# Kernel optimization log

Measured on AMD Instinct MI355X. Metric: run time of the kernel, lower is better.

## Reference

```python
import jax, jax.numpy as jnp
import numpy as np

B, L, C, H = 8, 1024, 384, 6
D = C // H          # head_dim = 64
K, N = 2, 4         # radial_degree, angular_degree
EPS = 1e-5


def setup_inputs() -> dict:
    key = jax.random.key(0)
    ks = jax.random.split(key, 8)
    x = jax.random.normal(ks[0], (B, L, C), dtype=jnp.float32)
    pos = jax.random.uniform(ks[1], (B, L, 2), dtype=jnp.float32) * 32.0
    w_norm = jnp.ones((C,), dtype=jnp.float32)
    w_in = jax.random.normal(ks[2], (3 * C, C), dtype=jnp.float32) * 0.02
    b_in = jnp.zeros((3 * C,), dtype=jnp.float32)
    w_out = jax.random.normal(ks[3], (C, C), dtype=jnp.float32) * 0.02
    b_out = jnp.zeros((C,), dtype=jnp.float32)
    b_coef = jax.random.normal(ks[4], (H, K + 1, N + 1), dtype=jnp.float32) * 0.01
    b_coef = b_coef.at[:, 1, 0].set(1.0)  # reset_parameters fills b[..., 1, 0] = 1
    c_coef = jax.random.normal(ks[5], (H, K + 1, N + 1), dtype=jnp.float32) * 0.01
    return {"x": x, "pos": pos, "w_norm": w_norm, "w_in": w_in, "b_in": b_in,
            "w_out": w_out, "b_out": b_out, "b_coef": b_coef, "c_coef": c_coef}


def _polar_bias(pos, b_coef, c_coef):
    # pos: (B, L, 2) -> bias grid (B, H, L, L)
    dist = pos[:, :, None, :] - pos[:, None, :, :]           # (B, Lq, Lk, 2)
    theta = jnp.arctan2(dist[..., 1], dist[..., 0])          # (B, Lq, Lk)
    r = jnp.sqrt(jnp.sum(dist * dist, axis=-1))              # (B, Lq, Lk)
    r_pow = r[..., None] ** jnp.arange(K + 1, dtype=r.dtype)           # (B, Lq, Lk, K+1)
    ang = theta[..., None] * jnp.arange(N + 1, dtype=theta.dtype)      # (B, Lq, Lk, N+1)
    cos_part = jnp.einsum('hkn,bijk,bijn->bhij', b_coef, r_pow, jnp.cos(ang))
    sin_part = jnp.einsum('hkn,bijk,bijn->bhij', c_coef, r_pow, jnp.sin(ang))
    return cos_part + sin_part


def reference(x, pos, w_norm, w_in, b_in, w_out, b_out, b_coef, c_coef):
    # RMSNorm
    ms = jnp.mean(x * x, axis=-1, keepdims=True)
    xn = x * jax.lax.rsqrt(ms + EPS) * w_norm
    # packed QKV projection
    qkv = xn @ w_in.T + b_in                                  # (B, L, 3C)
    q, k, v = jnp.split(qkv, 3, axis=-1)
    def heads(t):  # (B, L, C) -> (B, H, L, D)
        return t.reshape(B, L, H, D).transpose(0, 2, 1, 3)
    q, k, v = heads(q), heads(k), heads(v)
    bias = _polar_bias(pos, b_coef, c_coef)                   # (B, H, L, L)
    scores = jnp.einsum('bhqd,bhkd->bhqk', q, k) / jnp.sqrt(jnp.float32(D)) + bias
    attn = jax.nn.softmax(scores, axis=-1)
    o = jnp.einsum('bhqk,bhkd->bhqd', attn, v)                # (B, H, L, D)
    o = o.transpose(0, 2, 1, 3).reshape(B, L, C)
    return o @ w_out.T + b_out
```

## Files before the change

### kernel.cpp

```cpp
#include <hip/hip_runtime.h>

typedef unsigned int  u32;
typedef unsigned short u16;
typedef __attribute__((ext_vector_type(8))) short short8;
typedef __attribute__((ext_vector_type(4))) float f32x4;

__device__ __forceinline__ u16 f2bf(float x) {
  union { float f; u32 u; } un; un.f = x;
  u32 r = un.u + 0x7FFFu + ((un.u >> 16) & 1u);
  return (u16)(r >> 16);
}
__device__ __forceinline__ f32x4 mfma_bf16(short8 a, short8 b, f32x4 c) {
  return __builtin_amdgcn_mfma_f32_16x16x32_bf16(a, b, c, 0, 0, 0);
}

__global__ __launch_bounds__(256) void prep_kernel(
    const float* __restrict__ x, const float* __restrict__ w_norm,
    const float* __restrict__ w_in, const float* __restrict__ w_out,
    u16* __restrict__ xn, u16* __restrict__ winb, u16* __restrict__ woutb)
{
  int blk = blockIdx.x, t = threadIdx.x;
  if (blk < 2048) {
    int wv = t >> 6, lane = t & 63;
    int row = blk * 4 + wv;
    const float* xr = x + (size_t)row * 384;
    float v[6]; float ss = 0.f;
    #pragma unroll
    for (int i = 0; i < 6; i++) { v[i] = xr[lane + 64 * i]; ss += v[i] * v[i]; }
    #pragma unroll
    for (int off = 32; off > 0; off >>= 1) ss += __shfl_xor(ss, off);
    float rs = __builtin_amdgcn_rsqf(ss * (1.0f / 384.0f) + 1e-5f);
    #pragma unroll
    for (int i = 0; i < 6; i++) {
      float xv = v[i] * rs * w_norm[lane + 64 * i];
      xn[(size_t)row * 384 + lane + 64 * i] = f2bf(xv);
    }
  } else {
    int base = (blk - 2048) * 2048 + t * 8;
    #pragma unroll
    for (int j = 0; j < 8; j++) {
      int idx = base + j;
      if (idx < 442368) winb[idx] = f2bf(w_in[idx]);
      else              woutb[idx - 442368] = f2bf(w_out[idx - 442368]);
    }
  }
}

template<bool OUT_F32, bool QSCALE>
__global__ __launch_bounds__(256) void gemm_kernel(
    const u16* __restrict__ A, int lda,
    const u16* __restrict__ Bw, int ldb,
    const float* __restrict__ bias, void* __restrict__ outp, int ldc, int K)
{
  __shared__ __attribute__((aligned(16))) u16 As[128 * 72];
  __shared__ __attribute__((aligned(16))) u16 Bs[128 * 72];
  int t = threadIdx.x;
  int lane = t & 63, wv = t >> 6;
  int g = lane >> 4, cl = lane & 15;
  int row0 = blockIdx.x * 128, col0 = blockIdx.y * 128;
  int wm = (wv >> 1) * 64, wn = (wv & 1) * 64;
  f32x4 acc[4][4];
  #pragma unroll
  for (int i = 0; i < 4; i++)
    #pragma unroll
    for (int j = 0; j < 4; j++) acc[i][j] = (f32x4){0.f, 0.f, 0.f, 0.f};

  for (int k0 = 0; k0 < K; k0 += 64) {
    __syncthreads();
    #pragma unroll
    for (int j = 0; j < 4; j++) {
      int i = t + 256 * j;
      int r = i >> 3, ch = i & 7;
      *(uint4*)(&As[r * 72 + ch * 8]) =
          *(const uint4*)(A + (size_t)(row0 + r) * lda + k0 + ch * 8);
      *(uint4*)(&Bs[r * 72 + ch * 8]) =
          *(const uint4*)(Bw + (size_t)(col0 + r) * ldb + k0 + ch * 8);
    }
    __syncthreads();
    #pragma unroll
    for (int kh = 0; kh < 2; kh++) {
      short8 af[4], bfr[4];
      #pragma unroll
      for (int s = 0; s < 4; s++) {
        af[s]  = *(const short8*)(&As[(wm + s * 16 + cl) * 72 + kh * 32 + g * 8]);
        bfr[s] = *(const short8*)(&Bs[(wn + s * 16 + cl) * 72 + kh * 32 + g * 8]);
      }
      #pragma unroll
      for (int i = 0; i < 4; i++)
        #pragma unroll
        for (int j = 0; j < 4; j++)
          acc[i][j] = mfma_bf16(af[i], bfr[j], acc[i][j]);
    }
  }
  #pragma unroll
  for (int i = 0; i < 4; i++) {
    #pragma unroll
    for (int j = 0; j < 4; j++) {
      int colb = col0 + wn + j * 16 + cl;
      float bv = bias[colb];
      #pragma unroll
      for (int r = 0; r < 4; r++) {
        int rowb = row0 + wm + i * 16 + g * 4 + r;
        float v = acc[i][j][r] + bv;
        if (QSCALE) { if (colb < 384) v *= 0.125f; }
        if (OUT_F32) ((float*)outp)[(size_t)rowb * ldc + colb] = v;
        else ((u16*)outp)[(size_t)rowb * ldc + colb] = f2bf(v);
      }
    }
  }
}

__global__ __launch_bounds__(256) void attn_hybrid3(
    const u16* __restrict__ qkv, const float* __restrict__ pos,
    const float* __restrict__ bcf, const float* __restrict__ ccf,
    u16* __restrict__ obuf)
{
  __shared__ __attribute__((aligned(16))) float sbuf[64][68];
  __shared__ __attribute__((aligned(16))) u16 vsmem[64][72];
  int blk = blockIdx.x;
  int qt = blk & 15, h = (blk >> 4) % 6, b = blk / 96;
  int t = threadIdx.x, lane = t & 63, wv = t >> 6;
  int g = lane >> 4, cl = lane & 15;

  float bc[15], cc[15];
  #pragma unroll
  for (int i = 0; i < 15; i++) { bc[i] = bcf[h * 15 + i]; cc[i] = ccf[h * 15 + i]; }

  const u16* qbase = qkv + (size_t)(b * 1024 + qt * 64 + wv * 16 + cl) * 1152 + h * 64;
  short8 qf0 = *(const short8*)(qbase + g * 8);
  short8 qf1 = *(const short8*)(qbase + 32 + g * 8);

  float qx[4], qy[4];
  #pragma unroll
  for (int r = 0; r < 4; r++) {
    int qr = qt * 64 + wv * 16 + 4 * g + r;
    qx[r] = pos[(size_t)(b * 1024 + qr) * 2 + 0];
    qy[r] = pos[(size_t)(b * 1024 + qr) * 2 + 1];
  }

  f32x4 oa[4];
  #pragma unroll
  for (int d = 0; d < 4; d++) oa[d] = (f32x4){0.f, 0.f, 0.f, 0.f};
  float m_own = -1e30f, l_own = 0.f;

  const u16* kb = qkv + (size_t)b * 1024 * 1152 + 384 + h * 64;
  const u16* vsrc = qkv + (size_t)b * 1024 * 1152 + 768 + h * 64 + wv * 16;
  const float* pb = pos + (size_t)b * 2048;

  for (int k0 = 0; k0 < 1024; k0 += 64) {
    {
      const u16* vr = vsrc + (size_t)(k0 + lane) * 1152;
      uint4 w0 = *(const uint4*)(vr);
      uint4 w1 = *(const uint4*)(vr + 8);
      int vd = wv * 16;
      vsmem[vd + 0][lane] = (u16)(w0.x);  vsmem[vd + 1][lane] = (u16)(w0.x >> 16);
      vsmem[vd + 2][lane] = (u16)(w0.y);  vsmem[vd + 3][lane] = (u16)(w0.y >> 16);
      vsmem[vd + 4][lane] = (u16)(w0.z);  vsmem[vd + 5][lane] = (u16)(w0.z >> 16);
      vsmem[vd + 6][lane] = (u16)(w0.w);  vsmem[vd + 7][lane] = (u16)(w0.w >> 16);
      vsmem[vd + 8][lane] = (u16)(w1.x);  vsmem[vd + 9][lane] = (u16)(w1.x >> 16);
      vsmem[vd +10][lane] = (u16)(w1.y);  vsmem[vd +11][lane] = (u16)(w1.y >> 16);
      vsmem[vd +12][lane] = (u16)(w1.z);  vsmem[vd +13][lane] = (u16)(w1.z >> 16);
      vsmem[vd +14][lane] = (u16)(w1.w);  vsmem[vd +15][lane] = (u16)(w1.w >> 16);
    }
    f32x4 s[4];
    #pragma unroll
    for (int ks = 0; ks < 4; ks++) {
      const u16* kr = kb + (size_t)(k0 + ks * 16 + cl) * 1152;
      short8 kf0 = *(const short8*)(kr + g * 8);
      short8 kf1 = *(const short8*)(kr + 32 + g * 8);
      f32x4 z = (f32x4){0.f, 0.f, 0.f, 0.f};
      z = mfma_bf16(qf0, kf0, z);
      z = mfma_bf16(qf1, kf1, z);
      s[ks] = z;
    }
    #pragma unroll
    for (int ks = 0; ks < 4; ks++) {
      int kidx = k0 + ks * 16 + cl;
      float kx = pb[kidx * 2], ky = pb[kidx * 2 + 1];
      #pragma unroll
      for (int r = 0; r < 4; r++) {
        float dx = qx[r] - kx, dy = qy[r] - ky;
        float r2 = dx * dx + dy * dy;
        bool zz = !(r2 > 0.f);
        float ir = zz ? 0.f : __builtin_amdgcn_rsqf(r2);
        float rr = r2 * ir;
        float c1 = zz ? 1.f : dx * ir;
        float s1 = dy * ir;
        float c2 = c1*c1 - s1*s1, s2 = 2.f*c1*s1;
        float c3 = c1*c2 - s1*s2, s3 = s1*c2 + c1*s2;
        float c4 = c2*c2 - s2*s2, s4 = 2.f*c2*s2;
        float a0 = bc[0] + bc[1]*c1 + bc[2]*c2 + bc[3]*c3 + bc[4]*c4
                 + cc[1]*s1 + cc[2]*s2 + cc[3]*s3 + cc[4]*s4;
        float a1 = bc[5] + bc[6]*c1 + bc[7]*c2 + bc[8]*c3 + bc[9]*c4
                 + cc[6]*s1 + cc[7]*s2 + cc[8]*s3 + cc[9]*s4;
        float a2 = bc[10] + bc[11]*c1 + bc[12]*c2 + bc[13]*c3 + bc[14]*c4
                 + cc[11]*s1 + cc[12]*s2 + cc[13]*s3 + cc[14]*s4;
        sbuf[wv * 16 + 4 * g + r][ks * 16 + cl] =
            s[ks][r] + a0 + rr * (a1 + rr * a2);
      }
    }
    __syncthreads();
    {
      int rown = wv * 16 + (lane & 15), cb = (lane >> 4) * 16;
      float tmax = -1e30f;
      #pragma unroll
      for (int c = 0; c < 16; c++) tmax = fmaxf(tmax, sbuf[rown][cb + c]);
      tmax = fmaxf(tmax, __shfl_xor(tmax, 16));
      tmax = fmaxf(tmax, __shfl_xor(tmax, 32));
      float mn = fmaxf(m_own, tmax);
      float sc = __builtin_amdgcn_exp2f((m_own - mn) * 1.44269504f);
      m_own = mn;
      float mrow = __shfl(mn, cl);
      #pragma unroll
      for (int r = 0; r < 4; r++) {
        float scr = __shfl(sc, 4 * g + r);
        #pragma unroll
        for (int d = 0; d < 4; d++) oa[d][r] *= scr;
      }
      float psum = 0.f;
      union { u16 u[8]; short8 s8; } pk0, pk1;
      const float* srow = &sbuf[wv * 16 + cl][0];
      #pragma unroll
      for (int j = 0; j < 8; j++) {
        float p = __builtin_amdgcn_exp2f((srow[8 * g + j] - mrow) * 1.44269504f);
        psum += p; pk0.u[j] = f2bf(p);
      }
      #pragma unroll
      for (int j = 0; j < 8; j++) {
        float p = __builtin_amdgcn_exp2f((srow[32 + 8 * g + j] - mrow) * 1.44269504f);
        psum += p; pk1.u[j] = f2bf(p);
      }
      psum += __shfl_xor(psum, 16);
      psum += __shfl_xor(psum, 32);
      l_own = l_own * sc + psum;
      #pragma unroll
      for (int d = 0; d < 4; d++) {
        short8 vf0 = *(const short8*)(&vsmem[d * 16 + cl][g * 8]);
        short8 vf1 = *(const short8*)(&vsmem[d * 16 + cl][32 + g * 8]);
        oa[d] = mfma_bf16(pk0.s8, vf0, oa[d]);
        oa[d] = mfma_bf16(pk1.s8, vf1, oa[d]);
      }
    }
    __syncthreads();
  }
  float inv = __builtin_amdgcn_rcpf(l_own);
  #pragma unroll
  for (int r = 0; r < 4; r++) {
    float invr = __shfl(inv, 4 * g + r);
    int qr = qt * 64 + wv * 16 + 4 * g + r;
    #pragma unroll
    for (int d = 0; d < 4; d++) {
      obuf[(size_t)(b * 1024 + qr) * 384 + h * 64 + d * 16 + cl] =
          f2bf(oa[d][r] * invr);
    }
  }
}

extern "C" void kernel_launch(void* const* d_in, const int* in_sizes, int n_in,
                              void* d_out, int out_size, void* d_ws, size_t ws_size,
                              hipStream_t stream) {
  const float* x      = (const float*)d_in[0];
  const float* pos    = (const float*)d_in[1];
  const float* w_norm = (const float*)d_in[2];
  const float* w_in   = (const float*)d_in[3];
  const float* b_in   = (const float*)d_in[4];
  const float* w_out  = (const float*)d_in[5];
  const float* b_out  = (const float*)d_in[6];
  const float* b_coef = (const float*)d_in[7];
  const float* c_coef = (const float*)d_in[8];

  char* ws = (char*)d_ws;
  u16* xn    = (u16*)(ws + 0);
  u16* obuf  = (u16*)(ws + 0);
  u16* winb  = (u16*)(ws + 6291456);
  u16* woutb = (u16*)(ws + 7176192);
  u16* qkvb  = (u16*)(ws + 7471104);

  prep_kernel<<<2336, 256, 0, stream>>>(x, w_norm, w_in, w_out, xn, winb, woutb);
  gemm_kernel<false, true><<<dim3(64, 9), 256, 0, stream>>>(
      xn, 384, winb, 384, b_in, qkvb, 1152, 384);
  attn_hybrid3<<<768, 256, 0, stream>>>(qkvb, pos, b_coef, c_coef, obuf);
  gemm_kernel<true, false><<<dim3(64, 3), 256, 0, stream>>>(
      obuf, 384, woutb, 384, b_out, (float*)d_out, 384, 384);
}
```

Before: 159.4 us.

## Split attention key range across two wave groups and merge softmax partials

The attention kernel now runs 512 threads per block. Two groups of four waves each handle half of the key sequence for the same 64-query tile, and their running max, sum and output partials are merged through shared memory at the end. The block-to-(batch, head) mapping is also remapped so that neighbouring block IDs spread over different batch-head pairs, which may improve cache locality or XCD distribution. This doubles the waves available to hide latency, but costs more LDS per block and an extra merge step.

```diff
diff --git a/kernel.cpp b/kernel.cpp
--- a/kernel.cpp
+++ b/kernel.cpp
@@ -110,30 +110,38 @@
   }
 }
 
-__global__ __launch_bounds__(256) void attn_hybrid3(
+__global__ __launch_bounds__(512) void attn_hybrid4(
     const u16* __restrict__ qkv, const float* __restrict__ pos,
     const float* __restrict__ bcf, const float* __restrict__ ccf,
     u16* __restrict__ obuf)
 {
-  __shared__ __attribute__((aligned(16))) float sbuf[64][68];
-  __shared__ __attribute__((aligned(16))) u16 vsmem[64][72];
-  int blk = blockIdx.x;
-  int qt = blk & 15, h = (blk >> 4) % 6, b = blk / 96;
+  __shared__ __attribute__((aligned(16))) float sbuf[2][64][66];
+  __shared__ __attribute__((aligned(16))) u16 vsmem[2][64][72];
+  __shared__ float mlbuf[2][4][16];
+
+  int bid = blockIdx.x;
+  int xslot = bid & 7, rest = bid >> 3;
+  int qt = rest & 15, gdiv = rest >> 4;
+  int g48 = gdiv * 8 + xslot;
+  int b = g48 / 6, h = g48 - b * 6;
+
   int t = threadIdx.x, lane = t & 63, wv = t >> 6;
+  int strip = wv & 3, half = wv >> 2;
   int g = lane >> 4, cl = lane & 15;
 
   float bc[15], cc[15];
   #pragma unroll
   for (int i = 0; i < 15; i++) { bc[i] = bcf[h * 15 + i]; cc[i] = ccf[h * 15 + i]; }
 
-  const u16* qbase = qkv + (size_t)(b * 1024 + qt * 64 + wv * 16 + cl) * 1152 + h * 64;
+  const u16* qbase =
+      qkv + (size_t)(b * 1024 + qt * 64 + strip * 16 + cl) * 1152 + h * 64;
   short8 qf0 = *(const short8*)(qbase + g * 8);
   short8 qf1 = *(const short8*)(qbase + 32 + g * 8);
 
   float qx[4], qy[4];
   #pragma unroll
   for (int r = 0; r < 4; r++) {
-    int qr = qt * 64 + wv * 16 + 4 * g + r;
+    int qr = qt * 64 + strip * 16 + 4 * g + r;
     qx[r] = pos[(size_t)(b * 1024 + qr) * 2 + 0];
     qy[r] = pos[(size_t)(b * 1024 + qr) * 2 + 1];
   }
@@ -144,23 +152,24 @@
   float m_own = -1e30f, l_own = 0.f;
 
   const u16* kb = qkv + (size_t)b * 1024 * 1152 + 384 + h * 64;
-  const u16* vsrc = qkv + (size_t)b * 1024 * 1152 + 768 + h * 64 + wv * 16;
+  const u16* vsrc = qkv + (size_t)b * 1024 * 1152 + 768 + h * 64 + strip * 16;
   const float* pb = pos + (size_t)b * 2048;
 
-  for (int k0 = 0; k0 < 1024; k0 += 64) {
+  for (int kt = 0; kt < 512; kt += 64) {
+    int k0 = half * 512 + kt;
     {
       const u16* vr = vsrc + (size_t)(k0 + lane) * 1152;
       uint4 w0 = *(const uint4*)(vr);
       uint4 w1 = *(const uint4*)(vr + 8);
-      int vd = wv * 16;
-      vsmem[vd + 0][lane] = (u16)(w0.x);  vsmem[vd + 1][lane] = (u16)(w0.x >> 16);
-      vsmem[vd + 2][lane] = (u16)(w0.y);  vsmem[vd + 3][lane] = (u16)(w0.y >> 16);
-      vsmem[vd + 4][lane] = (u16)(w0.z);  vsmem[vd + 5][lane] = (u16)(w0.z >> 16);
-      vsmem[vd + 6][lane] = (u16)(w0.w);  vsmem[vd + 7][lane] = (u16)(w0.w >> 16);
-      vsmem[vd + 8][lane] = (u16)(w1.x);  vsmem[vd + 9][lane] = (u16)(w1.x >> 16);
-      vsmem[vd +10][lane] = (u16)(w1.y);  vsmem[vd +11][lane] = (u16)(w1.y >> 16);
-      vsmem[vd +12][lane] = (u16)(w1.z);  vsmem[vd +13][lane] = (u16)(w1.z >> 16);
-      vsmem[vd +14][lane] = (u16)(w1.w);  vsmem[vd +15][lane] = (u16)(w1.w >> 16);
+      int vd = strip * 16;
+      vsmem[half][vd + 0][lane] = (u16)(w0.x);  vsmem[half][vd + 1][lane] = (u16)(w0.x >> 16);
+      vsmem[half][vd + 2][lane] = (u16)(w0.y);  vsmem[half][vd + 3][lane] = (u16)(w0.y >> 16);
+      vsmem[half][vd + 4][lane] = (u16)(w0.z);  vsmem[half][vd + 5][lane] = (u16)(w0.z >> 16);
+      vsmem[half][vd + 6][lane] = (u16)(w0.w);  vsmem[half][vd + 7][lane] = (u16)(w0.w >> 16);
+      vsmem[half][vd + 8][lane] = (u16)(w1.x);  vsmem[half][vd + 9][lane] = (u16)(w1.x >> 16);
+      vsmem[half][vd +10][lane] = (u16)(w1.y);  vsmem[half][vd +11][lane] = (u16)(w1.y >> 16);
+      vsmem[half][vd +12][lane] = (u16)(w1.z);  vsmem[half][vd +13][lane] = (u16)(w1.z >> 16);
+      vsmem[half][vd +14][lane] = (u16)(w1.w);  vsmem[half][vd +15][lane] = (u16)(w1.w >> 16);
     }
     f32x4 s[4];
     #pragma unroll
@@ -195,22 +204,21 @@
                  + cc[6]*s1 + cc[7]*s2 + cc[8]*s3 + cc[9]*s4;
         float a2 = bc[10] + bc[11]*c1 + bc[12]*c2 + bc[13]*c3 + bc[14]*c4
                  + cc[11]*s1 + cc[12]*s2 + cc[13]*s3 + cc[14]*s4;
-        sbuf[wv * 16 + 4 * g + r][ks * 16 + cl] =
+        sbuf[half][strip * 16 + 4 * g + r][ks * 16 + cl] =
             s[ks][r] + a0 + rr * (a1 + rr * a2);
       }
     }
     __syncthreads();
     {
-      int rown = wv * 16 + (lane & 15), cb = (lane >> 4) * 16;
+      int rown = strip * 16 + cl, cb = g * 16;
       float tmax = -1e30f;
       #pragma unroll
-      for (int c = 0; c < 16; c++) tmax = fmaxf(tmax, sbuf[rown][cb + c]);
+      for (int c = 0; c < 16; c++) tmax = fmaxf(tmax, sbuf[half][rown][cb + c]);
       tmax = fmaxf(tmax, __shfl_xor(tmax, 16));
       tmax = fmaxf(tmax, __shfl_xor(tmax, 32));
       float mn = fmaxf(m_own, tmax);
       float sc = __builtin_amdgcn_exp2f((m_own - mn) * 1.44269504f);
       m_own = mn;
-      float mrow = __shfl(mn, cl);
       #pragma unroll
       for (int r = 0; r < 4; r++) {
         float scr = __shfl(sc, 4 * g + r);
@@ -219,15 +227,15 @@
       }
       float psum = 0.f;
       union { u16 u[8]; short8 s8; } pk0, pk1;
-      const float* srow = &sbuf[wv * 16 + cl][0];
+      const float* srow = &sbuf[half][strip * 16 + cl][0];
       #pragma unroll
       for (int j = 0; j < 8; j++) {
-        float p = __builtin_amdgcn_exp2f((srow[8 * g + j] - mrow) * 1.44269504f);
+        float p = __builtin_amdgcn_exp2f((srow[8 * g + j] - mn) * 1.44269504f);
         psum += p; pk0.u[j] = f2bf(p);
       }
       #pragma unroll
       for (int j = 0; j < 8; j++) {
-        float p = __builtin_amdgcn_exp2f((srow[32 + 8 * g + j] - mrow) * 1.44269504f);
+        float p = __builtin_amdgcn_exp2f((srow[32 + 8 * g + j] - mn) * 1.44269504f);
         psum += p; pk1.u[j] = f2bf(p);
       }
       psum += __shfl_xor(psum, 16);
@@ -235,23 +243,43 @@
       l_own = l_own * sc + psum;
       #pragma unroll
       for (int d = 0; d < 4; d++) {
-        short8 vf0 = *(const short8*)(&vsmem[d * 16 + cl][g * 8]);
-        short8 vf1 = *(const short8*)(&vsmem[d * 16 + cl][32 + g * 8]);
+        short8 vf0 = *(const short8*)(&vsmem[half][d * 16 + cl][g * 8]);
+        short8 vf1 = *(const short8*)(&vsmem[half][d * 16 + cl][32 + g * 8]);
         oa[d] = mfma_bf16(pk0.s8, vf0, oa[d]);
         oa[d] = mfma_bf16(pk1.s8, vf1, oa[d]);
       }
     }
     __syncthreads();
   }
-  float inv = __builtin_amdgcn_rcpf(l_own);
-  #pragma unroll
-  for (int r = 0; r < 4; r++) {
-    float invr = __shfl(inv, 4 * g + r);
-    int qr = qt * 64 + wv * 16 + 4 * g + r;
-    #pragma unroll
-    for (int d = 0; d < 4; d++) {
-      obuf[(size_t)(b * 1024 + qr) * 384 + h * 64 + d * 16 + cl] =
-          f2bf(oa[d][r] * invr);
+  float* o1 = &sbuf[0][0][0];
+  if (half == 1) {
+    if (lane < 16) { mlbuf[0][strip][lane] = m_own; mlbuf[1][strip][lane] = l_own; }
+    #pragma unroll
+    for (int r = 0; r < 4; r++) {
+      int row = 4 * g + r;
+      #pragma unroll
+      for (int d = 0; d < 4; d++)
+        o1[(strip * 16 + row) * 64 + d * 16 + cl] = oa[d][r];
+    }
+  }
+  __syncthreads();
+  if (half == 0) {
+    float m1 = mlbuf[0][strip][cl], l1 = mlbuf[1][strip][cl];
+    float M  = fmaxf(m_own, m1);
+    float f0 = __builtin_amdgcn_exp2f((m_own - M) * 1.44269504f);
+    float f1 = __builtin_amdgcn_exp2f((m1    - M) * 1.44269504f);
+    float linv = __builtin_amdgcn_rcpf(l_own * f0 + l1 * f1);
+    #pragma unroll
+    for (int r = 0; r < 4; r++) {
+      int row = 4 * g + r;
+      float f0r = __shfl(f0, row), f1r = __shfl(f1, row), invr = __shfl(linv, row);
+      int qr = qt * 64 + strip * 16 + row;
+      #pragma unroll
+      for (int d = 0; d < 4; d++) {
+        float val = (oa[d][r] * f0r +
+                     o1[(strip * 16 + row) * 64 + d * 16 + cl] * f1r) * invr;
+        obuf[(size_t)(b * 1024 + qr) * 384 + h * 64 + d * 16 + cl] = f2bf(val);
+      }
     }
   }
 }
@@ -279,7 +307,7 @@
   prep_kernel<<<2336, 256, 0, stream>>>(x, w_norm, w_in, w_out, xn, winb, woutb);
   gemm_kernel<false, true><<<dim3(64, 9), 256, 0, stream>>>(
       xn, 384, winb, 384, b_in, qkvb, 1152, 384);
-  attn_hybrid3<<<768, 256, 0, stream>>>(qkvb, pos, b_coef, c_coef, obuf);
+  attn_hybrid4<<<768, 512, 0, stream>>>(qkvb, pos, b_coef, c_coef, obuf);
   gemm_kernel<true, false><<<dim3(64, 3), 256, 0, stream>>>(
       obuf, 384, woutb, 384, b_out, (float*)d_out, 384, 384);
 }
```

Measured after the change: 167.1 us. 1.05x slower.
